# Kernel optimization log

Measured on AMD Instinct MI355X. Metric: run time of the kernel, lower is better.

Reference implementation:

```python
import jax, jax.numpy as jnp
import numpy as np

B, S, HID = 2, 2048, 4096
NH, NKV, HD = 32, 8, 128
SCALING = HD ** -0.5
Q_SIZE = NH * HD          # 4096
KV_SIZE = NKV * HD        # 1024
GROUPS = NH // NKV        # 4


def setup_inputs() -> dict:
    key = jax.random.key(0)
    ks = jax.random.split(key, 5)
    hidden_states = jax.random.normal(ks[0], (B, S, HID), dtype=jnp.float32)
    # Realistic rotary embeddings: cos/sin of position-dependent angles, HF layout [B, S, HD]
    inv_freq = 1.0 / (10000.0 ** (jnp.arange(0, HD, 2, dtype=jnp.float32) / HD))  # [HD/2]
    pos = jnp.arange(S, dtype=jnp.float32)
    freqs = pos[:, None] * inv_freq[None, :]                 # [S, HD/2]
    emb = jnp.concatenate([freqs, freqs], axis=-1)           # [S, HD]
    cos = jnp.broadcast_to(jnp.cos(emb), (B, S, HD))
    sin = jnp.broadcast_to(jnp.sin(emb), (B, S, HD))
    w_qkv = jax.random.normal(ks[1], (Q_SIZE + 2 * KV_SIZE, HID), dtype=jnp.float32) * (HID ** -0.5)
    w_o = jax.random.normal(ks[2], (HID, Q_SIZE), dtype=jnp.float32) * (Q_SIZE ** -0.5)
    return {"hidden_states": hidden_states, "cos": cos, "sin": sin, "w_qkv": w_qkv, "w_o": w_o}


def _rotate_half(x):
    x1, x2 = jnp.split(x, 2, axis=-1)
    return jnp.concatenate([-x2, x1], axis=-1)


def reference(hidden_states, cos, sin, w_qkv, w_o):
    b, s, _ = hidden_states.shape
    # Fused QKV projection (attention_bias=False for llama)
    qkv = jnp.einsum('bsh,oh->bso', hidden_states, w_qkv)    # [B, S, Q+2KV]
    q = qkv[..., :Q_SIZE].reshape(b, s, NH, HD).transpose(0, 2, 1, 3)                       # [B, NH, S, D]
    k = qkv[..., Q_SIZE:Q_SIZE + KV_SIZE].reshape(b, s, NKV, HD).transpose(0, 2, 1, 3)      # [B, NKV, S, D]
    v = qkv[..., Q_SIZE + KV_SIZE:].reshape(b, s, NKV, HD).transpose(0, 2, 1, 3)            # [B, NKV, S, D]
    # Rotary position embedding (HF apply_rotary_pos_emb, unsqueeze over heads)
    c = cos[:, None, :, :]
    sn = sin[:, None, :, :]
    q = q * c + _rotate_half(q) * sn
    k = k * c + _rotate_half(k) * sn
    # GQA: repeat KV heads across groups
    k = jnp.repeat(k, GROUPS, axis=1)   # [B, NH, S, D]
    v = jnp.repeat(v, GROUPS, axis=1)
    # Causal SDPA
    scores = jnp.einsum('bhqd,bhkd->bhqk', q, k) * SCALING
    causal = jnp.tril(jnp.ones((s, s), dtype=bool))
    scores = jnp.where(causal[None, None], scores, jnp.finfo(scores.dtype).min)
    attn = jax.nn.softmax(scores, axis=-1)
    out = jnp.einsum('bhqk,bhkd->bhqd', attn, v)             # [B, NH, S, D]
    out = out.transpose(0, 2, 1, 3).reshape(b, s, Q_SIZE)    # [B, S, HID]
    return jnp.einsum('bso,ho->bsh', out, w_o)
```

## Files before the change

kernel.cpp:

```cpp
#include <hip/hip_runtime.h>
#include <hip/hip_bf16.h>
#include <cstdint>

#define B_DIM 2
#define S_LEN 2048
#define HID 4096
#define NH 32
#define NKV 8
#define HD 128
#define QSZ (NH * HD)
#define KVSZ (NKV * HD)
#define QKVW (QSZ + 2 * KVSZ)
#define SCALING 0.08838834764831845f

typedef __bf16 bf16;
typedef __bf16 bf16x4 __attribute__((ext_vector_type(4)));
typedef __bf16 bf16x8 __attribute__((ext_vector_type(8)));
typedef float floatx4 __attribute__((ext_vector_type(4)));

typedef __attribute__((address_space(1))) void GV;
typedef __attribute__((address_space(3))) void SV;

#define BAR() __builtin_amdgcn_s_barrier()
#define SCHED_FENCE() __builtin_amdgcn_sched_barrier(0)

__global__ __launch_bounds__(256) void cvt3(const float* __restrict__ a, bf16* __restrict__ oa, int na4,
                                            const float* __restrict__ b, bf16* __restrict__ ob, int nb4,
                                            const float* __restrict__ c, bf16* __restrict__ oc, int nc4) {
    int total = na4 + nb4 + nc4;
    int stride = gridDim.x * blockDim.x;
    for (int i = blockIdx.x * blockDim.x + threadIdx.x; i < total; i += stride) {
        const float* src; bf16* dst; int j = i;
        if (j < na4) { src = a; dst = oa; }
        else if ((j -= na4) < nb4) { src = b; dst = ob; }
        else { j -= nb4; src = c; dst = oc; }
        float4 v = ((const float4*)src)[j];
        bf16x4 o;
        o[0] = (bf16)v.x; o[1] = (bf16)v.y; o[2] = (bf16)v.z; o[3] = (bf16)v.w;
        ((bf16x4*)dst)[j] = o;
    }
}

template <int MODE, typename OutT>
__global__ __launch_bounds__(512, 2) void gemm256(const bf16* __restrict__ A,
                                                  const bf16* __restrict__ Bm,
                                                  OutT* __restrict__ C,
                                                  bf16* __restrict__ Qo,
                                                  bf16* __restrict__ Ko,
                                                  bf16* __restrict__ Vo,
                                                  const float* __restrict__ cosp,
                                                  const float* __restrict__ sinp,
                                                  int M, int N, int K) {
    __shared__ __align__(16) char smem[131072];
    (void)M;
    int tiles_n = N >> 8;
    int nwg = gridDim.x;
    int bid = blockIdx.x;
    int wg = (bid & 7) * (nwg >> 3) + (bid >> 3);
    int bm = wg / tiles_n, bn = wg % tiles_n;
    int tid = threadIdx.x;
    int lane = tid & 63, w = tid >> 6;
    int l15 = lane & 15, lg = lane >> 4, l7 = l15 & 7;
    int wm = w >> 2, wn = w & 3;
    const bf16* Ab = A + (size_t)bm * 256 * K;
    const bf16* Bb = Bm + (size_t)bn * 256 * K;

    auto AsP = [&](int buf, int h) -> char* { return smem + (buf * 2 + h) * 16384; };
    auto BsP = [&](int buf, int h) -> char* { return smem + 65536 + (buf * 2 + h) * 16384; };

    int o_lo = tid * 16, o_hi = o_lo + 8192;
    int r_lo = o_lo >> 7, r_hi = o_hi >> 7;
    int eo0 = r_lo * K + ((((o_lo >> 4) & 7) ^ (r_lo & 7)) << 3);
    int eo1 = r_hi * K + ((((o_hi >> 4) & 7) ^ (r_hi & 7)) << 3);
    const bf16* AbH[2] = {Ab, Ab + (size_t)128 * K};
    const bf16* BbH[2] = {Bb, Bb + (size_t)128 * K};

    auto stageA = [&](int buf, int h, int kt) {
        const bf16* base = AbH[h] + kt * 64;
        __builtin_amdgcn_global_load_lds((GV*)(base + eo0), (SV*)(AsP(buf, h) + o_lo), 16, 0, 0);
        __builtin_amdgcn_global_load_lds((GV*)(base + eo1), (SV*)(AsP(buf, h) + o_hi), 16, 0, 0);
    };
    auto stageB = [&](int buf, int h, int kt) {
        const bf16* base = BbH[h] + kt * 64;
        __builtin_amdgcn_global_load_lds((GV*)(base + eo0), (SV*)(BsP(buf, h) + o_lo), 16, 0, 0);
        __builtin_amdgcn_global_load_lds((GV*)(base + eo1), (SV*)(BsP(buf, h) + o_hi), 16, 0, 0);
    };
    auto rdA = [&](int buf, int fr, int kk) -> bf16x8 {
        int off = (fr * 16 + l15) * 128 + ((((kk << 2) | lg) ^ l7) << 4);
        return *(const bf16x8*)(AsP(buf, wm) + off);
    };
    auto rdB = [&](int buf, int fc, int kk) -> bf16x8 {
        int off = ((wn & 1) * 64 + fc * 16 + l15) * 128 + ((((kk << 2) | lg) ^ l7) << 4);
        return *(const bf16x8*)(BsP(buf, wn >> 1) + off);
    };

    floatx4 acc[8][4] = {};
    bf16x8 aF[4][2], bF[4][2];
    int nk = K >> 6, niter = nk >> 1;

    stageA(0, 0, 0); stageA(0, 1, 0); stageB(0, 0, 0); stageB(0, 1, 0);
    stageB(1, 0, 1); stageB(1, 1, 1);
    asm volatile("s_waitcnt vmcnt(4)" ::: "memory");
    SCHED_FENCE();
    BAR();

    auto quad = [&](int ra, int ca) {
        __builtin_amdgcn_s_setprio(1);
#pragma unroll
        for (int fr = 0; fr < 4; ++fr)
#pragma unroll
            for (int fc = 0; fc < 2; ++fc)
#pragma unroll
                for (int kk = 0; kk < 2; ++kk)
                    acc[ra * 4 + fr][ca * 2 + fc] = __builtin_amdgcn_mfma_f32_16x16x32_bf16(
                        aF[fr][kk], bF[ca * 2 + fc][kk], acc[ra * 4 + fr][ca * 2 + fc], 0, 0, 0);
        __builtin_amdgcn_s_setprio(0);
    };

    for (int i = 0; i < niter; ++i) {
        bool nl = (i + 1 < niter);
        int kt1 = 2 * i + 1, kt2 = 2 * i + 2, kt3 = 2 * i + 3;
#pragma unroll
        for (int fr = 0; fr < 4; ++fr)
#pragma unroll
            for (int kk = 0; kk < 2; ++kk) aF[fr][kk] = rdA(0, fr, kk);
#pragma unroll
        for (int fc = 0; fc < 2; ++fc)
#pragma unroll
            for (int kk = 0; kk < 2; ++kk) bF[fc][kk] = rdB(0, fc, kk);
        stageA(1, 0, kt1);
        BAR(); quad(0, 0); BAR();
#pragma unroll
        for (int fc = 2; fc < 4; ++fc)
#pragma unroll
            for (int kk = 0; kk < 2; ++kk) bF[fc][kk] = rdB(0, fc, kk);
        stageA(1, 1, kt1);
        BAR(); quad(0, 1); BAR();
#pragma unroll
        for (int fr = 0; fr < 4; ++fr)
#pragma unroll
            for (int kk = 0; kk < 2; ++kk) aF[fr][kk] = rdA(0, 4 + fr, kk);
        if (nl) stageB(0, 0, kt2);
        BAR(); quad(1, 0); BAR();
        if (nl) stageB(0, 1, kt2);
        BAR(); quad(1, 1);
        if (nl) asm volatile("s_waitcnt vmcnt(4)" ::: "memory");
        else    asm volatile("s_waitcnt vmcnt(0)" ::: "memory");
        SCHED_FENCE();
        BAR();
#pragma unroll
        for (int fr = 0; fr < 4; ++fr)
#pragma unroll
            for (int kk = 0; kk < 2; ++kk) aF[fr][kk] = rdA(1, fr, kk);
#pragma unroll
        for (int fc = 0; fc < 2; ++fc)
#pragma unroll
            for (int kk = 0; kk < 2; ++kk) bF[fc][kk] = rdB(1, fc, kk);
        if (nl) stageA(0, 0, kt2);
        BAR(); quad(0, 0); BAR();
#pragma unroll
        for (int fc = 2; fc < 4; ++fc)
#pragma unroll
            for (int kk = 0; kk < 2; ++kk) bF[fc][kk] = rdB(1, fc, kk);
        if (nl) stageA(0, 1, kt2);
        BAR(); quad(0, 1); BAR();
#pragma unroll
        for (int fr = 0; fr < 4; ++fr)
#pragma unroll
            for (int kk = 0; kk < 2; ++kk) aF[fr][kk] = rdA(1, 4 + fr, kk);
        if (nl) stageB(1, 0, kt3);
        BAR(); quad(1, 0); BAR();
        if (nl) stageB(1, 1, kt3);
        BAR(); quad(1, 1);
        asm volatile("s_waitcnt vmcnt(4)" ::: "memory");
        SCHED_FENCE();
        BAR();
    }

    if constexpr (MODE == 0) {
        int brow = bm * 256 + wm * 128, bcol = bn * 256 + wn * 64;
#pragma unroll
        for (int fr = 0; fr < 8; ++fr)
#pragma unroll
            for (int fc = 0; fc < 4; ++fc) {
                int col = bcol + fc * 16 + l15;
#pragma unroll
                for (int r = 0; r < 4; ++r) {
                    int row = brow + fr * 16 + lg * 4 + r;
                    C[(size_t)row * N + col] = (OutT)acc[fr][fc][r];
                }
            }
    } else {
        __syncthreads();
        int b = (bm * 256) >> 11, s0 = (bm * 256) & (S_LEN - 1);
        int colb = wn * 64, rowb = wm * 128;
        if (bn < 20) {
            bf16* Cb = (bf16*)smem;
#pragma unroll
            for (int fr = 0; fr < 8; ++fr)
#pragma unroll
                for (int fc = 0; fc < 4; ++fc) {
                    int col = colb + fc * 16 + l15;
                    int br = rowb + fr * 16 + lg * 4;
#pragma unroll
                    for (int r = 0; r < 4; ++r) {
                        int row = br + r;
                        Cb[row * 256 + ((((col >> 3) ^ (row & 7)) << 3) | (col & 7))] =
                            (bf16)acc[fr][fc][r];
                    }
                }
            __syncthreads();
            bool isQ = (bn < 16);
            int hh = w & 1;
            int c = l15, d0 = c * 8;
            float scale = isQ ? SCALING : 1.0f;
            float sgn = (c < 8) ? -1.0f : 1.0f;
            bf16* Ob = isQ ? (Qo + ((size_t)(b * NH + bn * 2 + hh) * S_LEN) * HD)
                           : (Ko + ((size_t)(b * NKV + (bn - 16) * 2 + hh) * S_LEN) * HD);
            int slot_s = hh * 16 + c, slot_p = hh * 16 + (c ^ 8);
#pragma unroll
            for (int rd = 0; rd < 16; ++rd) {
                int row = (w >> 1) * 64 + rd * 4 + lg;
                int s = s0 + row;
                bf16x8 xs = *(const bf16x8*)(Cb + row * 256 + ((slot_s ^ (row & 7)) << 3));
                bf16x8 xp = *(const bf16x8*)(Cb + row * 256 + ((slot_p ^ (row & 7)) << 3));
                const float* cr = cosp + ((size_t)b * S_LEN + s) * HD + d0;
                const float* sr = sinp + ((size_t)b * S_LEN + s) * HD + d0;
                float4 c0 = *(const float4*)cr, c1 = *(const float4*)(cr + 4);
                float4 s0v = *(const float4*)sr, s1v = *(const float4*)(sr + 4);
                float cv[8] = {c0.x, c0.y, c0.z, c0.w, c1.x, c1.y, c1.z, c1.w};
                float sv[8] = {s0v.x, s0v.y, s0v.z, s0v.w, s1v.x, s1v.y, s1v.z, s1v.w};
                bf16x8 o;
#pragma unroll
                for (int e = 0; e < 8; ++e)
                    o[e] = (bf16)(((float)xs[e] * cv[e] + sgn * (float)xp[e] * sv[e]) * scale);
                *(bf16x8*)(Ob + (size_t)s * HD + d0) = o;
            }
        } else {
#pragma unroll
            for (int fr = 0; fr < 8; ++fr)
#pragma unroll
                for (int fc = 0; fc < 4; ++fc) {
                    int col = colb + fc * 16 + l15;
                    int br = rowb + fr * 16 + lg * 4;
#pragma unroll
                    for (int r = 0; r < 4; ++r) {
                        int row = br + r;
                        *(bf16*)(smem + col * 512 +
                                 (((((row >> 3) ^ (col & 7)) << 4) | ((row & 7) << 1)))) =
                            (bf16)acc[fr][fc][r];
                    }
                }
            __syncthreads();
            int kvb = (bn - 20) * 2;
            int sc = tid & 31;
            int dgr = tid >> 5;
#pragma unroll
            for (int j = 0; j < 16; ++j) {
                int col = dgr * 16 + j;
                int kv = kvb + (col >> 7), d = col & 127;
                bf16x8 o = *(const bf16x8*)(smem + col * 512 + ((sc ^ (col & 7)) << 4));
                *(bf16x8*)(Vo + ((size_t)(b * NKV + kv) * HD + d) * S_LEN + s0 + sc * 8) = o;
            }
        }
    }
}

__global__ __launch_bounds__(256, 2) void attn_fwd(const bf16* __restrict__ Q,
                                                   const bf16* __restrict__ K,
                                                   const bf16* __restrict__ Vt,
                                                   bf16* __restrict__ O) {
    __shared__ __align__(16) bf16 Ks[2][64 * 128];
    __shared__ __align__(16) bf16 Vs[128 * 64];
    __shared__ __align__(16) bf16 Ps[4][32 * 64];

    int ord = blockIdx.x;
    int qt = 15 - (ord >> 6);
    int bh = ord & 63;
    int h = bh & 31, b = bh >> 5;
    int kvh = h >> 2;
    int tid = threadIdx.x, lane = tid & 63, w = tid >> 6;
    int l15 = lane & 15, lg = lane >> 4, l7 = l15 & 7, lg4 = lg * 4;
    int q0 = qt * 128;
    int qbw = q0 + w * 32;

    const bf16* Qb = Q + ((size_t)(b * NH + h) * S_LEN) * HD;
    const bf16* Kb = K + ((size_t)(b * NKV + kvh) * S_LEN) * HD;
    const bf16* Vb = Vt + ((size_t)(b * NKV + kvh) * HD) * S_LEN;

    bf16x8 qf[2][4];
#pragma unroll
    for (int i = 0; i < 2; ++i)
#pragma unroll
        for (int ks = 0; ks < 4; ++ks)
            qf[i][ks] = *(const bf16x8*)(Qb + (size_t)(qbw + i * 16 + l15) * HD + ks * 32 + lg * 8);

    floatx4 accO[2][8] = {};
    float m_run[2] = {-1e30f, -1e30f}, l_run[2] = {0.f, 0.f};

    char* Pc = (char*)Ps[w];
    int nt = 2 * qt + 2;

    auto stageK = [&](int buf, int t) {
        int kv0 = t * 64;
#pragma unroll
        for (int it = 0; it < 4; ++it) {
            int o = it * 4096 + tid * 16;
            int r = o >> 8, pb = (o >> 4) & 15;
            int lb = pb ^ (r & 7);
            __builtin_amdgcn_global_load_lds((GV*)(Kb + (size_t)(kv0 + r) * HD + lb * 8),
                                             (SV*)((char*)Ks[buf] + o), 16, 0, 0);
        }
    };
    auto stageV = [&](int t) {
        int kv0 = t * 64;
#pragma unroll
        for (int it = 0; it < 4; ++it) {
            int o = it * 4096 + tid * 16;
            int d = o >> 7, pb = (o >> 4) & 7;
            int lb = pb ^ (d & 7);
            __builtin_amdgcn_global_load_lds((GV*)(Vb + (size_t)d * S_LEN + kv0 + lb * 8),
                                             (SV*)((char*)Vs + o), 16, 0, 0);
        }
    };

    stageK(0, 0);

    for (int t = 0; t < nt; ++t) {
        int cur = t & 1;
        int kv0 = t * 64;
        stageV(t);
        stageK(cur ^ 1, t + 1 < nt ? t + 1 : t);
        asm volatile("s_waitcnt vmcnt(8)" ::: "memory");
        SCHED_FENCE();
        BAR();

        const char* Kc = (const char*)Ks[cur];
        floatx4 s[2][4] = {};
        __builtin_amdgcn_s_setprio(1);
#pragma unroll
        for (int nm = 0; nm < 4; ++nm)
#pragma unroll
            for (int ks = 0; ks < 4; ++ks) {
                bf16x8 kf = *(const bf16x8*)(Kc + (nm * 16 + l15) * 256 +
                                             ((((ks << 2) | lg) ^ l7) << 4));
                s[0][nm] = __builtin_amdgcn_mfma_f32_16x16x32_bf16(kf, qf[0][ks], s[0][nm], 0, 0, 0);
                s[1][nm] = __builtin_amdgcn_mfma_f32_16x16x32_bf16(kf, qf[1][ks], s[1][nm], 0, 0, 0);
            }
        __builtin_amdgcn_s_setprio(0);

#pragma unroll
        for (int i = 0; i < 2; ++i) {
            if (kv0 + 63 > qbw + i * 16) {
                int qg = qbw + i * 16 + l15;
#pragma unroll
                for (int nm = 0; nm < 4; ++nm)
#pragma unroll
                    for (int r = 0; r < 4; ++r)
                        if (kv0 + nm * 16 + lg4 + r > qg) s[i][nm][r] = -1e30f;
            }
            float pm = -1e30f;
#pragma unroll
            for (int nm = 0; nm < 4; ++nm)
#pragma unroll
                for (int r = 0; r < 4; ++r) pm = fmaxf(pm, s[i][nm][r]);
            pm = fmaxf(pm, __shfl_xor(pm, 16));
            pm = fmaxf(pm, __shfl_xor(pm, 32));
            bool need = !__all(pm - m_run[i] <= 8.f);
            float corr = 1.f;
            if (need) {
                float mn = fmaxf(m_run[i], pm);
                corr = __expf(m_run[i] - mn);
                m_run[i] = mn;
            }
            float mn = m_run[i];
            float sum = 0.f;
#pragma unroll
            for (int nm = 0; nm < 4; ++nm) {
                bf16x4 pk;
#pragma unroll
                for (int r = 0; r < 4; ++r) {
                    float p = __expf(s[i][nm][r] - mn);
                    sum += p;
                    pk[r] = (bf16)p;
                }
                *(bf16x4*)(Pc + (i * 16 + l15) * 128 +
                           ((((nm << 1) | (lg >> 1)) ^ l7) << 4) + ((lg & 1) << 3)) = pk;
            }
            sum += __shfl_xor(sum, 16);
            sum += __shfl_xor(sum, 32);
            if (need) {
                l_run[i] = l_run[i] * corr + sum;
#pragma unroll
                for (int r = 0; r < 4; ++r) {
                    float cr = __shfl(corr, lg4 + r);
#pragma unroll
                    for (int g = 0; g < 8; ++g) accO[i][g][r] *= cr;
                }
            } else {
                l_run[i] += sum;
            }
        }

        asm volatile("s_waitcnt vmcnt(4)" ::: "memory");
        SCHED_FENCE();
        BAR();
        asm volatile("s_waitcnt lgkmcnt(0)" ::: "memory");
        SCHED_FENCE();

        bf16x8 pf[2][2];
#pragma unroll
        for (int i = 0; i < 2; ++i)
#pragma unroll
            for (int ks = 0; ks < 2; ++ks)
                pf[i][ks] = *(const bf16x8*)(Pc + (i * 16 + l15) * 128 +
                                             ((((ks << 2) | lg) ^ l7) << 4));
        __builtin_amdgcn_s_setprio(1);
#pragma unroll
        for (int g = 0; g < 8; ++g)
#pragma unroll
            for (int ks = 0; ks < 2; ++ks) {
                bf16x8 vf = *(const bf16x8*)((const char*)Vs + (g * 16 + l15) * 128 +
                                             ((((ks << 2) | lg) ^ l7) << 4));
                accO[0][g] = __builtin_amdgcn_mfma_f32_16x16x32_bf16(pf[0][ks], vf, accO[0][g], 0, 0, 0);
                accO[1][g] = __builtin_amdgcn_mfma_f32_16x16x32_bf16(pf[1][ks], vf, accO[1][g], 0, 0, 0);
            }
        __builtin_amdgcn_s_setprio(0);
        BAR();
    }

#pragma unroll
    for (int i = 0; i < 2; ++i) {
        float inv = 1.f / l_run[i];
#pragma unroll
        for (int r = 0; r < 4; ++r) {
            float vinv = __shfl(inv, lg4 + r);
            int qg = qbw + i * 16 + lg4 + r;
            size_t ob = ((size_t)(b * S_LEN + qg) * NH + h) * HD;
#pragma unroll
            for (int g = 0; g < 8; ++g)
                O[ob + g * 16 + l15] = (bf16)(accO[i][g][r] * vinv);
        }
    }
}

extern "C" void kernel_launch(void* const* d_in, const int* in_sizes, int n_in,
                              void* d_out, int out_size, void* d_ws, size_t ws_size,
                              hipStream_t stream) {
    const float* hs   = (const float*)d_in[0];
    const float* cosp = (const float*)d_in[1];
    const float* sinp = (const float*)d_in[2];
    const float* wqkv = (const float*)d_in[3];
    const float* wo   = (const float*)d_in[4];
    float* out = (float*)d_out;

    char* ws = (char*)d_ws;
    size_t off = 0;
    auto alloc = [&](size_t bytes) {
        char* p = ws + off;
        off += (bytes + 255) & ~(size_t)255;
        return p;
    };
    const size_t n_hs = (size_t)B_DIM * S_LEN * HID;
    const size_t n_wqkv = (size_t)QKVW * HID;
    const size_t n_wo = (size_t)HID * QSZ;

    bf16* hs_b   = (bf16*)alloc(n_hs * 2);
    bf16* wqkv_b = (bf16*)alloc(n_wqkv * 2);
    bf16* wo_b   = (bf16*)alloc(n_wo * 2);
    bf16* Qb  = (bf16*)alloc((size_t)B_DIM * NH * S_LEN * HD * 2);
    bf16* Kb  = (bf16*)alloc((size_t)B_DIM * NKV * S_LEN * HD * 2);
    bf16* Vtb = (bf16*)alloc((size_t)B_DIM * NKV * HD * S_LEN * 2);
    bf16* attn_b = hs_b;

    cvt3<<<2048, 256, 0, stream>>>(hs, hs_b, (int)(n_hs >> 2),
                                   wqkv, wqkv_b, (int)(n_wqkv >> 2),
                                   wo, wo_b, (int)(n_wo >> 2));

    gemm256<1, bf16><<<(4096 / 256) * (6144 / 256), 512, 0, stream>>>(
        hs_b, wqkv_b, (bf16*)nullptr, Qb, Kb, Vtb, cosp, sinp, B_DIM * S_LEN, QKVW, HID);

    attn_fwd<<<B_DIM * NH * (S_LEN / 128), 256, 0, stream>>>(Qb, Kb, Vtb, attn_b);

    gemm256<0, float><<<(4096 / 256) * (4096 / 256), 512, 0, stream>>>(
        attn_b, wo_b, out, nullptr, nullptr, nullptr, nullptr, nullptr,
        B_DIM * S_LEN, HID, HID);
}
```

Before: 478.2 us.

## Split QKV projection into dedicated 128x256-tile kernel with triple-buffered pipeline

Replaces the templated QKV mode of the shared GEMM with a dedicated kernel using 128-row tiles and a three-stage LDS ring buffer, doubling the workgroup count to improve wave balance and latency hiding. The RoPE and V-transpose epilogues are adapted to the smaller tile. The output GEMM is simplified to a plain store path. The larger LDS footprint limits occupancy, and smaller tiles raise per-flop global traffic.

```diff
diff --git a/kernel.cpp b/kernel.cpp
--- a/kernel.cpp
+++ b/kernel.cpp
@@ -41,17 +41,192 @@
     }
 }
 
-template <int MODE, typename OutT>
+__global__ __launch_bounds__(512, 2) void gemm_qkv(const bf16* __restrict__ A,
+                                                   const bf16* __restrict__ Bm,
+                                                   bf16* __restrict__ Qo,
+                                                   bf16* __restrict__ Ko,
+                                                   bf16* __restrict__ Vo,
+                                                   const float* __restrict__ cosp,
+                                                   const float* __restrict__ sinp) {
+    __shared__ __align__(16) char smem[147456];
+    const int K = HID;
+    int nwg = gridDim.x;
+    int bid = blockIdx.x;
+    int wg = (bid & 7) * (nwg >> 3) + (bid >> 3);
+    int bm = wg / 24, bn = wg % 24;
+    int tid = threadIdx.x;
+    int lane = tid & 63, w = tid >> 6;
+    int l15 = lane & 15, lg = lane >> 4, l7 = l15 & 7;
+    int wm = w >> 2, wn = w & 3;
+    const bf16* Ab = A + (size_t)bm * 128 * K;
+    const bf16* Bb = Bm + (size_t)bn * 256 * K;
+
+    auto AsP = [&](int buf) -> char* { return smem + buf * 16384; };
+    auto BsP = [&](int buf) -> char* { return smem + 49152 + buf * 32768; };
+
+    int oL[4], eB[4];
+#pragma unroll
+    for (int l = 0; l < 4; ++l) {
+        int o = tid * 16 + l * 8192;
+        int r = o >> 7;
+        oL[l] = o;
+        eB[l] = r * K + ((((o >> 4) & 7) ^ (r & 7)) << 3);
+    }
+
+    auto stageA = [&](int buf, int kt) {
+        const bf16* base = Ab + kt * 64;
+        __builtin_amdgcn_global_load_lds((GV*)(base + eB[0]), (SV*)(AsP(buf) + oL[0]), 16, 0, 0);
+        __builtin_amdgcn_global_load_lds((GV*)(base + eB[1]), (SV*)(AsP(buf) + oL[1]), 16, 0, 0);
+    };
+    auto stageBh = [&](int buf, int h, int kt) {
+        const bf16* base = Bb + kt * 64;
+        int l0 = 2 * h;
+        __builtin_amdgcn_global_load_lds((GV*)(base + eB[l0]), (SV*)(BsP(buf) + oL[l0]), 16, 0, 0);
+        __builtin_amdgcn_global_load_lds((GV*)(base + eB[l0 + 1]), (SV*)(BsP(buf) + oL[l0 + 1]), 16, 0, 0);
+    };
+    auto rdA = [&](int buf, int fr, int kk) -> bf16x8 {
+        int off = (wm * 64 + fr * 16 + l15) * 128 + ((((kk << 2) | lg) ^ l7) << 4);
+        return *(const bf16x8*)(AsP(buf) + off);
+    };
+    auto rdB = [&](int buf, int fc, int kk) -> bf16x8 {
+        int off = (wn >> 1) * 16384 + ((wn & 1) * 64 + fc * 16 + l15) * 128 +
+                  ((((kk << 2) | lg) ^ l7) << 4);
+        return *(const bf16x8*)(BsP(buf) + off);
+    };
+
+    floatx4 acc[4][4] = {};
+    bf16x8 aF[4][2], bF[2][2];
+    const int nk = K >> 6;
+
+    stageA(0, 0); stageBh(0, 0, 0); stageBh(0, 1, 0);
+    stageA(1, 1); stageBh(1, 0, 1); stageBh(1, 1, 1);
+    asm volatile("s_waitcnt vmcnt(6)" ::: "memory");
+    SCHED_FENCE();
+    BAR();
+
+    auto quad = [&](int ca) {
+        __builtin_amdgcn_s_setprio(1);
+#pragma unroll
+        for (int fr = 0; fr < 4; ++fr)
+#pragma unroll
+            for (int fc = 0; fc < 2; ++fc)
+#pragma unroll
+                for (int kk = 0; kk < 2; ++kk)
+                    acc[fr][ca * 2 + fc] = __builtin_amdgcn_mfma_f32_16x16x32_bf16(
+                        aF[fr][kk], bF[fc][kk], acc[fr][ca * 2 + fc], 0, 0, 0);
+        __builtin_amdgcn_s_setprio(0);
+    };
+
+    int cur = 0;
+    for (int kt = 0; kt < nk; ++kt) {
+        int nxt = cur + 2; if (nxt >= 3) nxt -= 3;
+        bool pf = (kt + 2 < nk);
+#pragma unroll
+        for (int fr = 0; fr < 4; ++fr)
+#pragma unroll
+            for (int kk = 0; kk < 2; ++kk) aF[fr][kk] = rdA(cur, fr, kk);
+#pragma unroll
+        for (int fc = 0; fc < 2; ++fc)
+#pragma unroll
+            for (int kk = 0; kk < 2; ++kk) bF[fc][kk] = rdB(cur, fc, kk);
+        if (pf) { stageA(nxt, kt + 2); stageBh(nxt, 0, kt + 2); }
+        BAR();
+        quad(0);
+        BAR();
+#pragma unroll
+        for (int fc = 0; fc < 2; ++fc)
+#pragma unroll
+            for (int kk = 0; kk < 2; ++kk) bF[fc][kk] = rdB(cur, 2 + fc, kk);
+        if (pf) stageBh(nxt, 1, kt + 2);
+        BAR();
+        quad(1);
+        if (pf) asm volatile("s_waitcnt vmcnt(6)" ::: "memory");
+        else    asm volatile("s_waitcnt vmcnt(0)" ::: "memory");
+        SCHED_FENCE();
+        BAR();
+        cur = cur + 1; if (cur >= 3) cur = 0;
+    }
+
+    __syncthreads();
+    int b = (bm * 128) >> 11, s0 = (bm * 128) & (S_LEN - 1);
+    int colb = wn * 64, rowb = wm * 64;
+    if (bn < 20) {
+        bf16* Cb = (bf16*)smem;
+#pragma unroll
+        for (int fr = 0; fr < 4; ++fr)
+#pragma unroll
+            for (int fc = 0; fc < 4; ++fc) {
+                int col = colb + fc * 16 + l15;
+                int br = rowb + fr * 16 + lg * 4;
+#pragma unroll
+                for (int r = 0; r < 4; ++r) {
+                    int row = br + r;
+                    Cb[row * 256 + ((((col >> 3) ^ (row & 7)) << 3) | (col & 7))] =
+                        (bf16)acc[fr][fc][r];
+                }
+            }
+        __syncthreads();
+        bool isQ = (bn < 16);
+        int hh = w & 1;
+        int c = l15, d0 = c * 8;
+        float scale = isQ ? SCALING : 1.0f;
+        float sgn = (c < 8) ? -1.0f : 1.0f;
+        bf16* Ob = isQ ? (Qo + ((size_t)(b * NH + bn * 2 + hh) * S_LEN) * HD)
+                       : (Ko + ((size_t)(b * NKV + (bn - 16) * 2 + hh) * S_LEN) * HD);
+        int slot_s = hh * 16 + c, slot_p = hh * 16 + (c ^ 8);
+#pragma unroll
+        for (int rd = 0; rd < 8; ++rd) {
+            int row = (w >> 1) * 32 + rd * 4 + lg;
+            int s = s0 + row;
+            bf16x8 xs = *(const bf16x8*)(Cb + row * 256 + ((slot_s ^ (row & 7)) << 3));
+            bf16x8 xp = *(const bf16x8*)(Cb + row * 256 + ((slot_p ^ (row & 7)) << 3));
+            const float* cr = cosp + ((size_t)b * S_LEN + s) * HD + d0;
+            const float* sr = sinp + ((size_t)b * S_LEN + s) * HD + d0;
+            float4 c0 = *(const float4*)cr, c1 = *(const float4*)(cr + 4);
+            float4 s0v = *(const float4*)sr, s1v = *(const float4*)(sr + 4);
+            float cv[8] = {c0.x, c0.y, c0.z, c0.w, c1.x, c1.y, c1.z, c1.w};
+            float sv[8] = {s0v.x, s0v.y, s0v.z, s0v.w, s1v.x, s1v.y, s1v.z, s1v.w};
+            bf16x8 o;
+#pragma unroll
+            for (int e = 0; e < 8; ++e)
+                o[e] = (bf16)(((float)xs[e] * cv[e] + sgn * (float)xp[e] * sv[e]) * scale);
+            *(bf16x8*)(Ob + (size_t)s * HD + d0) = o;
+        }
+    } else {
+#pragma unroll
+        for (int fr = 0; fr < 4; ++fr)
+#pragma unroll
+            for (int fc = 0; fc < 4; ++fc) {
+                int col = colb + fc * 16 + l15;
+                int br = rowb + fr * 16 + lg * 4;
+#pragma unroll
+                for (int r = 0; r < 4; ++r) {
+                    int row = br + r;
+                    *(bf16*)(smem + col * 256 +
+                             (((((row >> 3) ^ (col & 7)) << 4) | ((row & 7) << 1)))) =
+                        (bf16)acc[fr][fc][r];
+                }
+            }
+        __syncthreads();
+        int kvb = (bn - 20) * 2;
+        int sc = tid & 15;
+        int dgr = tid >> 4;
+#pragma unroll
+        for (int j = 0; j < 8; ++j) {
+            int col = dgr * 8 + j;
+            int kv = kvb + (col >> 7), d = col & 127;
+            bf16x8 o = *(const bf16x8*)(smem + col * 256 + ((sc ^ (col & 7)) << 4));
+            *(bf16x8*)(Vo + ((size_t)(b * NKV + kv) * HD + d) * S_LEN + s0 + sc * 8) = o;
+        }
+    }
+}
+
+template <typename OutT>
 __global__ __launch_bounds__(512, 2) void gemm256(const bf16* __restrict__ A,
                                                   const bf16* __restrict__ Bm,
-                                                  OutT* __restrict__ C,
-                                                  bf16* __restrict__ Qo,
-                                                  bf16* __restrict__ Ko,
-                                                  bf16* __restrict__ Vo,
-                                                  const float* __restrict__ cosp,
-                                                  const float* __restrict__ sinp,
-                                                  int M, int N, int K) {
-    __shared__ __align__(16) char smem[131072];
+                                                  OutT* __restrict__ C, int M, int N, int K) {
+    __shared__ __align__(16) bf16 As[2][2][128 * 64];
+    __shared__ __align__(16) bf16 Bs[2][2][128 * 64];
     (void)M;
     int tiles_n = N >> 8;
     int nwg = gridDim.x;
@@ -65,9 +240,6 @@
     const bf16* Ab = A + (size_t)bm * 256 * K;
     const bf16* Bb = Bm + (size_t)bn * 256 * K;
 
-    auto AsP = [&](int buf, int h) -> char* { return smem + (buf * 2 + h) * 16384; };
-    auto BsP = [&](int buf, int h) -> char* { return smem + 65536 + (buf * 2 + h) * 16384; };
-
     int o_lo = tid * 16, o_hi = o_lo + 8192;
     int r_lo = o_lo >> 7, r_hi = o_hi >> 7;
     int eo0 = r_lo * K + ((((o_lo >> 4) & 7) ^ (r_lo & 7)) << 3);
@@ -77,21 +249,21 @@
 
     auto stageA = [&](int buf, int h, int kt) {
         const bf16* base = AbH[h] + kt * 64;
-        __builtin_amdgcn_global_load_lds((GV*)(base + eo0), (SV*)(AsP(buf, h) + o_lo), 16, 0, 0);
-        __builtin_amdgcn_global_load_lds((GV*)(base + eo1), (SV*)(AsP(buf, h) + o_hi), 16, 0, 0);
+        __builtin_amdgcn_global_load_lds((GV*)(base + eo0), (SV*)((char*)As[buf][h] + o_lo), 16, 0, 0);
+        __builtin_amdgcn_global_load_lds((GV*)(base + eo1), (SV*)((char*)As[buf][h] + o_hi), 16, 0, 0);
     };
     auto stageB = [&](int buf, int h, int kt) {
         const bf16* base = BbH[h] + kt * 64;
-        __builtin_amdgcn_global_load_lds((GV*)(base + eo0), (SV*)(BsP(buf, h) + o_lo), 16, 0, 0);
-        __builtin_amdgcn_global_load_lds((GV*)(base + eo1), (SV*)(BsP(buf, h) + o_hi), 16, 0, 0);
+        __builtin_amdgcn_global_load_lds((GV*)(base + eo0), (SV*)((char*)Bs[buf][h] + o_lo), 16, 0, 0);
+        __builtin_amdgcn_global_load_lds((GV*)(base + eo1), (SV*)((char*)Bs[buf][h] + o_hi), 16, 0, 0);
     };
     auto rdA = [&](int buf, int fr, int kk) -> bf16x8 {
         int off = (fr * 16 + l15) * 128 + ((((kk << 2) | lg) ^ l7) << 4);
-        return *(const bf16x8*)(AsP(buf, wm) + off);
+        return *(const bf16x8*)((const char*)As[buf][wm] + off);
     };
     auto rdB = [&](int buf, int fc, int kk) -> bf16x8 {
         int off = ((wn & 1) * 64 + fc * 16 + l15) * 128 + ((((kk << 2) | lg) ^ l7) << 4);
-        return *(const bf16x8*)(BsP(buf, wn >> 1) + off);
+        return *(const bf16x8*)((const char*)Bs[buf][wn >> 1] + off);
     };
 
     floatx4 acc[8][4] = {};
@@ -177,93 +349,18 @@
         BAR();
     }
 
-    if constexpr (MODE == 0) {
-        int brow = bm * 256 + wm * 128, bcol = bn * 256 + wn * 64;
-#pragma unroll
-        for (int fr = 0; fr < 8; ++fr)
-#pragma unroll
-            for (int fc = 0; fc < 4; ++fc) {
-                int col = bcol + fc * 16 + l15;
-#pragma unroll
-                for (int r = 0; r < 4; ++r) {
-                    int row = brow + fr * 16 + lg * 4 + r;
-                    C[(size_t)row * N + col] = (OutT)acc[fr][fc][r];
-                }
-            }
-    } else {
-        __syncthreads();
-        int b = (bm * 256) >> 11, s0 = (bm * 256) & (S_LEN - 1);
-        int colb = wn * 64, rowb = wm * 128;
-        if (bn < 20) {
-            bf16* Cb = (bf16*)smem;
-#pragma unroll
-            for (int fr = 0; fr < 8; ++fr)
-#pragma unroll
-                for (int fc = 0; fc < 4; ++fc) {
-                    int col = colb + fc * 16 + l15;
-                    int br = rowb + fr * 16 + lg * 4;
-#pragma unroll
-                    for (int r = 0; r < 4; ++r) {
-                        int row = br + r;
-                        Cb[row * 256 + ((((col >> 3) ^ (row & 7)) << 3) | (col & 7))] =
-                            (bf16)acc[fr][fc][r];
-                    }
-                }
-            __syncthreads();
-            bool isQ = (bn < 16);
-            int hh = w & 1;
-            int c = l15, d0 = c * 8;
-            float scale = isQ ? SCALING : 1.0f;
-            float sgn = (c < 8) ? -1.0f : 1.0f;
-            bf16* Ob = isQ ? (Qo + ((size_t)(b * NH + bn * 2 + hh) * S_LEN) * HD)
-                           : (Ko + ((size_t)(b * NKV + (bn - 16) * 2 + hh) * S_LEN) * HD);
-            int slot_s = hh * 16 + c, slot_p = hh * 16 + (c ^ 8);
-#pragma unroll
-            for (int rd = 0; rd < 16; ++rd) {
-                int row = (w >> 1) * 64 + rd * 4 + lg;
-                int s = s0 + row;
-                bf16x8 xs = *(const bf16x8*)(Cb + row * 256 + ((slot_s ^ (row & 7)) << 3));
-                bf16x8 xp = *(const bf16x8*)(Cb + row * 256 + ((slot_p ^ (row & 7)) << 3));
-                const float* cr = cosp + ((size_t)b * S_LEN + s) * HD + d0;
-                const float* sr = sinp + ((size_t)b * S_LEN + s) * HD + d0;
-                float4 c0 = *(const float4*)cr, c1 = *(const float4*)(cr + 4);
-                float4 s0v = *(const float4*)sr, s1v = *(const float4*)(sr + 4);
-                float cv[8] = {c0.x, c0.y, c0.z, c0.w, c1.x, c1.y, c1.z, c1.w};
-                float sv[8] = {s0v.x, s0v.y, s0v.z, s0v.w, s1v.x, s1v.y, s1v.z, s1v.w};
-                bf16x8 o;
-#pragma unroll
-                for (int e = 0; e < 8; ++e)
-                    o[e] = (bf16)(((float)xs[e] * cv[e] + sgn * (float)xp[e] * sv[e]) * scale);
-                *(bf16x8*)(Ob + (size_t)s * HD + d0) = o;
-            }
-        } else {
-#pragma unroll
-            for (int fr = 0; fr < 8; ++fr)
-#pragma unroll
-                for (int fc = 0; fc < 4; ++fc) {
-                    int col = colb + fc * 16 + l15;
-                    int br = rowb + fr * 16 + lg * 4;
-#pragma unroll
-                    for (int r = 0; r < 4; ++r) {
-                        int row = br + r;
-                        *(bf16*)(smem + col * 512 +
-                                 (((((row >> 3) ^ (col & 7)) << 4) | ((row & 7) << 1)))) =
-                            (bf16)acc[fr][fc][r];
-                    }
-                }
-            __syncthreads();
-            int kvb = (bn - 20) * 2;
-            int sc = tid & 31;
-            int dgr = tid >> 5;
-#pragma unroll
-            for (int j = 0; j < 16; ++j) {
-                int col = dgr * 16 + j;
-                int kv = kvb + (col >> 7), d = col & 127;
-                bf16x8 o = *(const bf16x8*)(smem + col * 512 + ((sc ^ (col & 7)) << 4));
-                *(bf16x8*)(Vo + ((size_t)(b * NKV + kv) * HD + d) * S_LEN + s0 + sc * 8) = o;
-            }
-        }
-    }
+    int brow = bm * 256 + wm * 128, bcol = bn * 256 + wn * 64;
+#pragma unroll
+    for (int fr = 0; fr < 8; ++fr)
+#pragma unroll
+        for (int fc = 0; fc < 4; ++fc) {
+            int col = bcol + fc * 16 + l15;
+#pragma unroll
+            for (int r = 0; r < 4; ++r) {
+                int row = brow + fr * 16 + lg * 4 + r;
+                C[(size_t)row * N + col] = (OutT)acc[fr][fc][r];
+            }
+        }
 }
 
 __global__ __launch_bounds__(256, 2) void attn_fwd(const bf16* __restrict__ Q,
@@ -477,12 +574,11 @@
                                    wqkv, wqkv_b, (int)(n_wqkv >> 2),
                                    wo, wo_b, (int)(n_wo >> 2));
 
-    gemm256<1, bf16><<<(4096 / 256) * (6144 / 256), 512, 0, stream>>>(
-        hs_b, wqkv_b, (bf16*)nullptr, Qb, Kb, Vtb, cosp, sinp, B_DIM * S_LEN, QKVW, HID);
+    gemm_qkv<<<(4096 / 128) * (QKVW / 256), 512, 0, stream>>>(
+        hs_b, wqkv_b, Qb, Kb, Vtb, cosp, sinp);
 
     attn_fwd<<<B_DIM * NH * (S_LEN / 128), 256, 0, stream>>>(Qb, Kb, Vtb, attn_b);
 
-    gemm256<0, float><<<(4096 / 256) * (4096 / 256), 512, 0, stream>>>(
-        attn_b, wo_b, out, nullptr, nullptr, nullptr, nullptr, nullptr,
-        B_DIM * S_LEN, HID, HID);
+    gemm256<float><<<(4096 / 256) * (4096 / 256), 512, 0, stream>>>(
+        attn_b, wo_b, out, B_DIM * S_LEN, HID, HID);
 }
```

New measurement: 495.7 us. 3.7% more time.

## Double-buffer V tiles in LDS and drop mid-iteration barrier in attention

Applied to the files above, without the earlier changes.

V is now staged into two LDS buffers alongside K, so tile t+1's K and V are both prefetched while tile t is computed. This removes the per-iteration wait and barrier between the softmax and the PV matmul that previously waited for V to land. The row-max reduction is also rewritten as a balanced tree. The cost is 16KB more shared memory per block, which could pressure occupancy at two blocks per CU.

```diff
diff --git a/kernel.cpp b/kernel.cpp
--- a/kernel.cpp
+++ b/kernel.cpp
@@ -271,7 +271,7 @@
                                                    const bf16* __restrict__ Vt,
                                                    bf16* __restrict__ O) {
     __shared__ __align__(16) bf16 Ks[2][64 * 128];
-    __shared__ __align__(16) bf16 Vs[128 * 64];
+    __shared__ __align__(16) bf16 Vs[2][128 * 64];
     __shared__ __align__(16) bf16 Ps[4][32 * 64];
 
     int ord = blockIdx.x;
@@ -312,7 +312,7 @@
                                              (SV*)((char*)Ks[buf] + o), 16, 0, 0);
         }
     };
-    auto stageV = [&](int t) {
+    auto stageV = [&](int buf, int t) {
         int kv0 = t * 64;
 #pragma unroll
         for (int it = 0; it < 4; ++it) {
@@ -320,22 +320,25 @@
             int d = o >> 7, pb = (o >> 4) & 7;
             int lb = pb ^ (d & 7);
             __builtin_amdgcn_global_load_lds((GV*)(Vb + (size_t)d * S_LEN + kv0 + lb * 8),
-                                             (SV*)((char*)Vs + o), 16, 0, 0);
+                                             (SV*)((char*)Vs[buf] + o), 16, 0, 0);
         }
     };
 
     stageK(0, 0);
+    stageV(0, 0);
 
     for (int t = 0; t < nt; ++t) {
         int cur = t & 1;
         int kv0 = t * 64;
-        stageV(t);
-        stageK(cur ^ 1, t + 1 < nt ? t + 1 : t);
-        asm volatile("s_waitcnt vmcnt(8)" ::: "memory");
+        bool more = (t + 1 < nt);
+        if (more) { stageK(cur ^ 1, t + 1); stageV(cur ^ 1, t + 1); }
+        if (more) asm volatile("s_waitcnt vmcnt(8)" ::: "memory");
+        else      asm volatile("s_waitcnt vmcnt(0)" ::: "memory");
         SCHED_FENCE();
         BAR();
 
         const char* Kc = (const char*)Ks[cur];
+        const char* Vc = (const char*)Vs[cur];
         floatx4 s[2][4] = {};
         __builtin_amdgcn_s_setprio(1);
 #pragma unroll
@@ -359,11 +362,11 @@
                     for (int r = 0; r < 4; ++r)
                         if (kv0 + nm * 16 + lg4 + r > qg) s[i][nm][r] = -1e30f;
             }
-            float pm = -1e30f;
-#pragma unroll
-            for (int nm = 0; nm < 4; ++nm)
-#pragma unroll
-                for (int r = 0; r < 4; ++r) pm = fmaxf(pm, s[i][nm][r]);
+            float t0 = fmaxf(fmaxf(s[i][0][0], s[i][0][1]), fmaxf(s[i][0][2], s[i][0][3]));
+            float t1 = fmaxf(fmaxf(s[i][1][0], s[i][1][1]), fmaxf(s[i][1][2], s[i][1][3]));
+            float t2 = fmaxf(fmaxf(s[i][2][0], s[i][2][1]), fmaxf(s[i][2][2], s[i][2][3]));
+            float t3 = fmaxf(fmaxf(s[i][3][0], s[i][3][1]), fmaxf(s[i][3][2], s[i][3][3]));
+            float pm = fmaxf(fmaxf(t0, t1), fmaxf(t2, t3));
             pm = fmaxf(pm, __shfl_xor(pm, 16));
             pm = fmaxf(pm, __shfl_xor(pm, 32));
             bool need = !__all(pm - m_run[i] <= 8.f);
@@ -402,9 +405,6 @@
             }
         }
 
-        asm volatile("s_waitcnt vmcnt(4)" ::: "memory");
-        SCHED_FENCE();
-        BAR();
         asm volatile("s_waitcnt lgkmcnt(0)" ::: "memory");
         SCHED_FENCE();
 
@@ -420,7 +420,7 @@
         for (int g = 0; g < 8; ++g)
 #pragma unroll
             for (int ks = 0; ks < 2; ++ks) {
-                bf16x8 vf = *(const bf16x8*)((const char*)Vs + (g * 16 + l15) * 128 +
+                bf16x8 vf = *(const bf16x8*)(Vc + (g * 16 + l15) * 128 +
                                              ((((ks << 2) | lg) ^ l7) << 4));
                 accO[0][g] = __builtin_amdgcn_mfma_f32_16x16x32_bf16(pf[0][ks], vf, accO[0][g], 0, 0, 0);
                 accO[1][g] = __builtin_amdgcn_mfma_f32_16x16x32_bf16(pf[1][ks], vf, accO[1][g], 0, 0, 0);
```

After: 481.0 us. No clear change (+0.6%).
